# Performance work log

Measured on AMD Instinct MI355X. Metric: run time of the kernel, lower is better.

## Reference

```python
import jax, jax.numpy as jnp
import numpy as np

N_HEADS = 4
HEAD_DIM = 128
FMAP_H, FMAP_W = 32, 32
IN_DIM = 512
BATCH = 16


def setup_inputs() -> dict:
    key = jax.random.key(0)
    k1, k2, k3, k4 = jax.random.split(key, 4)
    scale = HEAD_DIM ** (-0.5)
    x = jax.random.normal(k1, (BATCH, IN_DIM, FMAP_H, FMAP_W), dtype=jnp.float32)
    # 1x1 conv weight producing q,k,v stacked along output channels
    conv_w = jax.random.normal(k2, (3 * N_HEADS * HEAD_DIM, IN_DIM), dtype=jnp.float32) * (IN_DIM ** -0.5)
    pos_h = jax.random.normal(k3, (FMAP_H, HEAD_DIM), dtype=jnp.float32) * scale
    pos_w = jax.random.normal(k4, (FMAP_W, HEAD_DIM), dtype=jnp.float32) * scale
    return {"x": x, "conv_w": conv_w, "pos_h": pos_h, "pos_w": pos_w}


def reference(x, conv_w, pos_h, pos_w):
    B, C, H, W = x.shape
    hw = H * W
    scale = HEAD_DIM ** (-0.5)
    # 1x1 conv == pointwise linear over channels
    qkv = jnp.einsum('bchw,oc->bohw', x, conv_w)               # [B, 3*nh*hd, H, W]
    qkv = qkv.reshape(B, 3, N_HEADS, HEAD_DIM, hw)             # chunk + per-head split
    q = jnp.swapaxes(qkv[:, 0], -1, -2) * scale                # [B, nh, hw, hd]
    k = jnp.swapaxes(qkv[:, 1], -1, -2)
    v = jnp.swapaxes(qkv[:, 2], -1, -2)
    # absolute positional embedding: h[i,:]+w[j,:] flattened over positions
    emb = (pos_h[:, None, :] + pos_w[None, :, :]).reshape(hw, HEAD_DIM)
    sim = jnp.einsum('bhid,bhjd->bhij', q, k) + jnp.einsum('bhid,jd->bhij', q, emb)
    attn = jax.nn.softmax(sim, axis=-1)
    out = jnp.einsum('bhij,bhjd->bhid', attn, v)               # [B, nh, hw, hd]
    out = jnp.swapaxes(out, -1, -2)                            # [B, nh, hd, hw]
    return out.reshape(B, N_HEADS * HEAD_DIM, hw // N_HEADS, N_HEADS)
```

## Files before the change

kernel.cpp:

```cpp
#include <hip/hip_runtime.h>

#define NB 16
#define NH 4
#define HD 128
#define HW 1024
#define CIN 512

typedef short s16x8 __attribute__((ext_vector_type(8)));
typedef short s16x4 __attribute__((ext_vector_type(4)));
typedef float f32x4 __attribute__((ext_vector_type(4)));

static __device__ __forceinline__ short f2bf(float f) {
    union { float f; unsigned u; } v; v.f = f;
    unsigned r = v.u + 0x7fffu + ((v.u >> 16) & 1u);
    return (short)(r >> 16);
}

__global__ __launch_bounds__(256) void prep_xw(
    const float* __restrict__ x, const float* __restrict__ w,
    short* __restrict__ xT, short* __restrict__ Wb)
{
    int blk = blockIdx.x;
    if (blk < NB * 16 * 32) {
        int b = blk >> 9, rem = blk & 511;
        int ct = rem >> 5, pt = rem & 31;
        __shared__ float tile[32][33];
        int tc = threadIdx.x >> 5;
        int tp = threadIdx.x & 31;
        const float* xb = x + ((size_t)b * CIN + ct * 32) * HW + pt * 32;
        #pragma unroll
        for (int i = 0; i < 4; i++)
            tile[tc + i * 8][tp] = xb[(size_t)(tc + i * 8) * HW + tp];
        __syncthreads();
        int p = threadIdx.x >> 3, cq = threadIdx.x & 7;
        short* xo = xT + ((size_t)b * HW + pt * 32 + p) * CIN + ct * 32 + cq * 4;
        s16x4 o4 = { f2bf(tile[cq * 4 + 0][p]), f2bf(tile[cq * 4 + 1][p]),
                     f2bf(tile[cq * 4 + 2][p]), f2bf(tile[cq * 4 + 3][p]) };
        *reinterpret_cast<s16x4*>(xo) = o4;
    } else {
        int wb = blk - NB * 16 * 32;
        size_t base = (size_t)wb * 1024 + threadIdx.x * 4;
        const float4 v = *reinterpret_cast<const float4*>(w + base);
        s16x4 o4 = { f2bf(v.x), f2bf(v.y), f2bf(v.z), f2bf(v.w) };
        *reinterpret_cast<s16x4*>(Wb + base) = o4;
    }
}

__global__ __launch_bounds__(256, 3) void qkv_proj(
    const short* __restrict__ xT, const short* __restrict__ Wb,
    const float* __restrict__ pos_h, const float* __restrict__ pos_w,
    short* __restrict__ Q, short* __restrict__ Kp, short* __restrict__ Vt)
{
    __shared__ __align__(16) char smem[34816];
    short* As = (short*)smem;
    short* Bs = As + 128 * 64;
    short* vb = (short*)smem;

    const int pt = blockIdx.x, ot = blockIdx.y, b = blockIdx.z;
    const int tid = threadIdx.x;
    const int wave = tid >> 6, lane = tid & 63;
    const int l16 = lane & 15, quad = lane >> 4;
    const int wm = (wave & 1) * 64, wn = (wave >> 1) * 64;
    const int o0 = ot * 128, p0 = pt * 128;

    const short* xb = xT + (size_t)b * HW * CIN;

    const int r0 = tid >> 3, c0 = tid & 7;
    const int sphys = c0 ^ (r0 & 7);
    const short* wp = Wb + (size_t)(o0 + r0) * CIN + c0 * 8;
    const short* xp = xb + (size_t)(p0 + r0) * CIN + c0 * 8;
    short* adst = As + r0 * 64 + sphys * 8;
    short* bdst = Bs + r0 * 64 + sphys * 8;

    f32x4 acc[4][4];
    #pragma unroll
    for (int i = 0; i < 4; i++)
        #pragma unroll
        for (int j = 0; j < 4; j++)
            acc[i][j] = f32x4{0.f, 0.f, 0.f, 0.f};

    s16x8 wreg[4], xreg[4];
    #pragma unroll
    for (int p = 0; p < 4; p++) {
        wreg[p] = *(const s16x8*)(wp + (size_t)(p * 32) * CIN);
        xreg[p] = *(const s16x8*)(xp + (size_t)(p * 32) * CIN);
    }

    #pragma unroll 1
    for (int kc = 0; kc < CIN; kc += 64) {
        #pragma unroll
        for (int p = 0; p < 4; p++) {
            *(s16x8*)(adst + p * 32 * 64) = wreg[p];
            *(s16x8*)(bdst + p * 32 * 64) = xreg[p];
        }
        __syncthreads();
        int kcn = (kc + 64) & (CIN - 1);
        #pragma unroll
        for (int p = 0; p < 4; p++) {
            wreg[p] = *(const s16x8*)(wp + kcn + (size_t)(p * 32) * CIN);
            xreg[p] = *(const s16x8*)(xp + kcn + (size_t)(p * 32) * CIN);
        }
        #pragma unroll
        for (int kk = 0; kk < 2; kk++) {
            s16x8 aF[4], bF[4];
            #pragma unroll
            for (int mi = 0; mi < 4; mi++)
                aF[mi] = *(const s16x8*)(As + (wm + mi * 16 + l16) * 64
                                         + (((kk * 4 + quad) ^ (l16 & 7)) * 8));
            #pragma unroll
            for (int ni = 0; ni < 4; ni++)
                bF[ni] = *(const s16x8*)(Bs + (wn + ni * 16 + l16) * 64
                                         + (((kk * 4 + quad) ^ (l16 & 7)) * 8));
            #pragma unroll
            for (int mi = 0; mi < 4; mi++)
                #pragma unroll
                for (int ni = 0; ni < 4; ni++)
                    acc[mi][ni] = __builtin_amdgcn_mfma_f32_16x16x32_bf16(
                        aF[mi], bF[ni], acc[mi][ni], 0, 0, 0);
        }
        __syncthreads();
    }

    const int s = ot >> 2, h = ot & 3;
    const size_t bh = (size_t)(b * NH + h);

    if (s == 0) {
        const float qs = 0.08838834764831845f * 1.4426950408889634f;
        short* Qb = Q + bh * (size_t)(HW * HD);
        #pragma unroll
        for (int mi = 0; mi < 4; mi++) {
            int d0 = wm + mi * 16 + quad * 4;
            #pragma unroll
            for (int ni = 0; ni < 4; ni++) {
                int p = p0 + wn + ni * 16 + l16;
                f32x4 a = acc[mi][ni];
                s16x4 o4 = { f2bf(a.x * qs), f2bf(a.y * qs),
                             f2bf(a.z * qs), f2bf(a.w * qs) };
                *reinterpret_cast<s16x4*>(Qb + (size_t)p * HD + d0) = o4;
            }
        }
    } else if (s == 1) {
        short* Kb = Kp + bh * (size_t)(HW * HD);
        #pragma unroll
        for (int mi = 0; mi < 4; mi++) {
            int d0 = wm + mi * 16 + quad * 4;
            #pragma unroll
            for (int ni = 0; ni < 4; ni++) {
                int p = p0 + wn + ni * 16 + l16;
                const float4 eh = *reinterpret_cast<const float4*>(pos_h + (p >> 5) * HD + d0);
                const float4 ew = *reinterpret_cast<const float4*>(pos_w + (p & 31) * HD + d0);
                f32x4 a = acc[mi][ni];
                s16x4 o4 = { f2bf(a.x + eh.x + ew.x), f2bf(a.y + eh.y + ew.y),
                             f2bf(a.z + eh.z + ew.z), f2bf(a.w + eh.w + ew.w) };
                *reinterpret_cast<s16x4*>(Kb + (size_t)p * HD + d0) = o4;
            }
        }
    } else {
        __syncthreads();
        #pragma unroll
        for (int mi = 0; mi < 4; mi++) {
            int d0 = wm + mi * 16 + quad * 4;
            #pragma unroll
            for (int ni = 0; ni < 4; ni++) {
                int p = wn + ni * 16 + l16;
                f32x4 a = acc[mi][ni];
                vb[(d0 + 0) * 136 + p] = f2bf(a.x);
                vb[(d0 + 1) * 136 + p] = f2bf(a.y);
                vb[(d0 + 2) * 136 + p] = f2bf(a.z);
                vb[(d0 + 3) * 136 + p] = f2bf(a.w);
            }
        }
        __syncthreads();
        short* Vb = Vt + bh * (size_t)(HD * HW);
        int d = tid >> 1, half = tid & 1;
        #pragma unroll
        for (int j = 0; j < 8; j++) {
            s16x8 v8 = *(const s16x8*)(vb + d * 136 + half * 64 + j * 8);
            *reinterpret_cast<s16x8*>(Vb + (size_t)d * HW + p0 + half * 64 + j * 8) = v8;
        }
    }
}

__global__ __launch_bounds__(256, 2) void attn_fused(
    const short* __restrict__ Q, const short* __restrict__ Kp,
    const short* __restrict__ Vt, float* __restrict__ out)
{
    __shared__ __align__(16) short Ks[2][64 * 128];
    __shared__ __align__(16) short Vs[2][128 * 64];
    __shared__ __align__(16) short Ps[4][32 * 40];

    const int flat = blockIdx.x;
    const int qt = flat >> 6;
    const int bh = flat & 63;
    const int tid = threadIdx.x;
    const int wave = tid >> 6, lane = tid & 63;
    const int l16 = lane & 15, quad = lane >> 4;

    const short* Qb = Q + (size_t)bh * (HW * HD);
    const short* Kb = Kp + (size_t)bh * (HW * HD);
    const short* Vb = Vt + (size_t)bh * (HD * HW);
    short* myP = Ps[wave];

    const int q0 = qt * 128 + wave * 32;

    s16x8 bQ[2][4];
    #pragma unroll
    for (int nt = 0; nt < 2; nt++)
        #pragma unroll
        for (int kk = 0; kk < 4; kk++)
            bQ[nt][kk] = *(const s16x8*)(Qb + (size_t)(q0 + nt * 16 + l16) * HD
                                         + kk * 32 + quad * 8);

    s16x8 ones;
    #pragma unroll
    for (int j = 0; j < 8; j++) ones[j] = (short)0x3F80;

    f32x4 Oacc[2][8];
    #pragma unroll
    for (int mt = 0; mt < 2; mt++)
        #pragma unroll
        for (int dt = 0; dt < 8; dt++)
            Oacc[mt][dt] = f32x4{0.f, 0.f, 0.f, 0.f};
    f32x4 lacc[2] = { f32x4{0.f, 0.f, 0.f, 0.f}, f32x4{0.f, 0.f, 0.f, 0.f} };

    const int kKey = tid >> 4, kC = tid & 15;
    const int kPhys = kC ^ kKey;
    const short* kgp = Kb + (size_t)kKey * HD + kC * 8;
    const int kOff = kKey * 128 + kPhys * 8;
    const int vD = tid >> 3, vC = tid & 7;
    const int vPhys = vC ^ (vD & 7);
    const short* vgp = Vb + (size_t)vD * HW + vC * 8;
    const int vOff = vD * 64 + vPhys * 8;

    s16x8 kreg[4], vreg[4];
    #pragma unroll
    for (int i = 0; i < 4; i++) {
        kreg[i] = *(const s16x8*)(kgp + (size_t)(i * 16) * HD);
        vreg[i] = *(const s16x8*)(vgp + (size_t)(i * 32) * HW);
    }
    #pragma unroll
    for (int i = 0; i < 4; i++) {
        *(s16x8*)(&Ks[0][kOff] + i * 16 * 128) = kreg[i];
        *(s16x8*)(&Vs[0][vOff] + i * 32 * 64) = vreg[i];
    }
    #pragma unroll
    for (int i = 0; i < 4; i++) {
        kreg[i] = *(const s16x8*)(kgp + (size_t)(64 + i * 16) * HD);
        vreg[i] = *(const s16x8*)(vgp + 64 + (size_t)(i * 32) * HW);
    }
    __syncthreads();

    #pragma unroll 1
    for (int kt = 0; kt < 16; kt++) {
        const int cur = kt & 1, nxt = cur ^ 1;
        const short* ks = Ks[cur];
        const short* vs = Vs[cur];

        #pragma unroll
        for (int i = 0; i < 4; i++) {
            *(s16x8*)(&Ks[nxt][kOff] + i * 16 * 128) = kreg[i];
            *(s16x8*)(&Vs[nxt][vOff] + i * 32 * 64) = vreg[i];
        }
        int ktn = (kt + 2) & 15;
        #pragma unroll
        for (int i = 0; i < 4; i++) {
            kreg[i] = *(const s16x8*)(kgp + (size_t)(ktn * 64 + i * 16) * HD);
            vreg[i] = *(const s16x8*)(vgp + ktn * 64 + (size_t)(i * 32) * HW);
        }

        f32x4 c[4][2];
        __builtin_amdgcn_s_setprio(1);
        #pragma unroll
        for (int mtp = 0; mtp < 4; mtp++) {
            s16x8 aK[4];
            #pragma unroll
            for (int kk = 0; kk < 4; kk++)
                aK[kk] = *(const s16x8*)(ks + (mtp * 16 + l16) * 128
                                         + (((kk * 4 + quad) ^ l16) * 8));
            c[mtp][0] = f32x4{0.f, 0.f, 0.f, 0.f};
            c[mtp][1] = f32x4{0.f, 0.f, 0.f, 0.f};
            #pragma unroll
            for (int kk = 0; kk < 4; kk++) {
                c[mtp][0] = __builtin_amdgcn_mfma_f32_16x16x32_bf16(
                    aK[kk], bQ[0][kk], c[mtp][0], 0, 0, 0);
                c[mtp][1] = __builtin_amdgcn_mfma_f32_16x16x32_bf16(
                    aK[kk], bQ[1][kk], c[mtp][1], 0, 0, 0);
            }
        }
        __builtin_amdgcn_s_setprio(0);

        #pragma unroll
        for (int h = 0; h < 2; h++) {
            #pragma unroll
            for (int m2 = 0; m2 < 2; m2++)
                #pragma unroll
                for (int nt = 0; nt < 2; nt++) {
                    f32x4 pv = c[h * 2 + m2][nt];
                    s16x4 pp = { f2bf(__builtin_amdgcn_exp2f(pv[0])),
                                 f2bf(__builtin_amdgcn_exp2f(pv[1])),
                                 f2bf(__builtin_amdgcn_exp2f(pv[2])),
                                 f2bf(__builtin_amdgcn_exp2f(pv[3])) };
                    int q = nt * 16 + l16;
                    *(s16x4*)(myP + q * 40 + m2 * 16 + quad * 4) = pp;
                }

            s16x8 aP[2];
            #pragma unroll
            for (int mt = 0; mt < 2; mt++)
                aP[mt] = *(const s16x8*)(myP + (mt * 16 + l16) * 40 + quad * 8);

            __builtin_amdgcn_s_setprio(1);
            #pragma unroll
            for (int mt = 0; mt < 2; mt++)
                lacc[mt] = __builtin_amdgcn_mfma_f32_16x16x32_bf16(
                    aP[mt], ones, lacc[mt], 0, 0, 0);

            #pragma unroll
            for (int dt = 0; dt < 8; dt++) {
                s16x8 bV = *(const s16x8*)(vs + (dt * 16 + l16) * 64
                                           + (((h * 4 + quad) ^ (l16 & 7)) * 8));
                #pragma unroll
                for (int mt = 0; mt < 2; mt++)
                    Oacc[mt][dt] = __builtin_amdgcn_mfma_f32_16x16x32_bf16(
                        aP[mt], bV, Oacc[mt][dt], 0, 0, 0);
            }
            __builtin_amdgcn_s_setprio(0);
        }
        __syncthreads();
    }

    float* ob = out + (size_t)bh * (HD * HW);
    #pragma unroll
    for (int mt = 0; mt < 2; mt++) {
        float inv[4];
        #pragma unroll
        for (int r = 0; r < 4; r++) inv[r] = __builtin_amdgcn_rcpf(lacc[mt][r]);
        int prow = q0 + mt * 16 + quad * 4;
        #pragma unroll
        for (int dt = 0; dt < 8; dt++) {
            int d = dt * 16 + l16;
            f32x4 o = Oacc[mt][dt];
            float4 o4 = { o[0] * inv[0], o[1] * inv[1],
                          o[2] * inv[2], o[3] * inv[3] };
            *reinterpret_cast<float4*>(ob + (size_t)d * HW + prow) = o4;
        }
    }
}

extern "C" void kernel_launch(void* const* d_in, const int* in_sizes, int n_in,
                              void* d_out, int out_size, void* d_ws, size_t ws_size,
                              hipStream_t stream) {
    const float* x  = (const float*)d_in[0];
    const float* w  = (const float*)d_in[1];
    const float* ph = (const float*)d_in[2];
    const float* pw = (const float*)d_in[3];

    const size_t BHPD = (size_t)NB * NH * HW * HD;
    short* Q    = (short*)d_ws;
    short* Kp   = Q + BHPD;
    short* Vt   = Kp + BHPD;
    short* xT   = Vt + BHPD;
    short* Wb   = xT + (size_t)NB * HW * CIN;
    float* outp = (float*)d_out;

    prep_xw<<<dim3(NB * 16 * 32 + 768), 256, 0, stream>>>(x, w, xT, Wb);
    qkv_proj<<<dim3(8, 12, NB), 256, 0, stream>>>(xT, Wb, ph, pw, Q, Kp, Vt);
    attn_fused<<<dim3(512), 256, 0, stream>>>(Q, Kp, Vt, outp);
}
```

Baseline: 175.5 us.

## Keep softmax probabilities in registers by permuting V key order

Removes the per-wave LDS staging buffer for exponentiated scores. The S^T MFMA accumulators are packed directly into the A operand of the PV MFMA, which uses a permuted key ordering. The V transpose in the projection kernel is changed to write keys in that same permuted order so the contraction stays correct. This saves LDS stores and loads and the associated latency per tile, at the cost of a slightly more complex V store pattern.

```diff
diff --git a/kernel.cpp b/kernel.cpp
--- a/kernel.cpp
+++ b/kernel.cpp
@@ -175,7 +175,12 @@
         int d = tid >> 1, half = tid & 1;
         #pragma unroll
         for (int j = 0; j < 8; j++) {
-            s16x8 v8 = *(const s16x8*)(vb + d * 136 + half * 64 + j * 8);
+            const short* row = vb + d * 136;
+            int base = (half * 2 + (j >> 2)) * 32 + (j & 3) * 4;
+            s16x4 lo = *(const s16x4*)(row + base);
+            s16x4 hi = *(const s16x4*)(row + base + 16);
+            s16x8 v8 = { lo[0], lo[1], lo[2], lo[3],
+                         hi[0], hi[1], hi[2], hi[3] };
             *reinterpret_cast<s16x8*>(Vb + (size_t)d * HW + p0 + half * 64 + j * 8) = v8;
         }
     }
@@ -187,7 +192,6 @@
 {
     __shared__ __align__(16) short Ks[2][64 * 128];
     __shared__ __align__(16) short Vs[2][128 * 64];
-    __shared__ __align__(16) short Ps[4][32 * 40];
 
     const int flat = blockIdx.x;
     const int qt = flat >> 6;
@@ -199,7 +203,6 @@
     const short* Qb = Q + (size_t)bh * (HW * HD);
     const short* Kb = Kp + (size_t)bh * (HW * HD);
     const short* Vb = Vt + (size_t)bh * (HD * HW);
-    short* myP = Ps[wave];
 
     const int q0 = qt * 128 + wave * 32;
 
@@ -291,23 +294,20 @@
 
         #pragma unroll
         for (int h = 0; h < 2; h++) {
-            #pragma unroll
-            for (int m2 = 0; m2 < 2; m2++)
-                #pragma unroll
-                for (int nt = 0; nt < 2; nt++) {
-                    f32x4 pv = c[h * 2 + m2][nt];
-                    s16x4 pp = { f2bf(__builtin_amdgcn_exp2f(pv[0])),
-                                 f2bf(__builtin_amdgcn_exp2f(pv[1])),
-                                 f2bf(__builtin_amdgcn_exp2f(pv[2])),
-                                 f2bf(__builtin_amdgcn_exp2f(pv[3])) };
-                    int q = nt * 16 + l16;
-                    *(s16x4*)(myP + q * 40 + m2 * 16 + quad * 4) = pp;
-                }
-
             s16x8 aP[2];
             #pragma unroll
-            for (int mt = 0; mt < 2; mt++)
-                aP[mt] = *(const s16x8*)(myP + (mt * 16 + l16) * 40 + quad * 8);
+            for (int mt = 0; mt < 2; mt++) {
+                f32x4 e0 = c[2 * h][mt], e1 = c[2 * h + 1][mt];
+                aP[mt] = s16x8{
+                    f2bf(__builtin_amdgcn_exp2f(e0[0])),
+                    f2bf(__builtin_amdgcn_exp2f(e0[1])),
+                    f2bf(__builtin_amdgcn_exp2f(e0[2])),
+                    f2bf(__builtin_amdgcn_exp2f(e0[3])),
+                    f2bf(__builtin_amdgcn_exp2f(e1[0])),
+                    f2bf(__builtin_amdgcn_exp2f(e1[1])),
+                    f2bf(__builtin_amdgcn_exp2f(e1[2])),
+                    f2bf(__builtin_amdgcn_exp2f(e1[3])) };
+            }
 
             __builtin_amdgcn_s_setprio(1);
             #pragma unroll
```

After: 167.0 us. 1.05x faster.
